# Kernel optimization log

Measured on AMD Instinct MI355X. Metric: run time of the kernel, lower is better.

## Reference

```python
import jax, jax.numpy as jnp
import numpy as np

N, D = 8192, 256
ALPHA, BETA, K = 50.0, 1.0, 2


def setup_inputs() -> dict:
    key = jax.random.key(0)
    k1, k2, k3, k4 = jax.random.split(key, 4)
    Q = jax.random.normal(k1, (N, D), dtype=jnp.float32)
    # 0/1 similarity structure; diagonal forced nonzero so no row is fully masked
    sim = jax.random.randint(k2, (N, N), 0, 2).astype(jnp.float32)
    sim = sim.at[jnp.arange(N), jnp.arange(N)].set(1.0)
    # nn.Linear(in_dim, in_dim) params: y = x @ W.T + b
    bound = 1.0 / np.sqrt(D)
    W = jax.random.uniform(k3, (D, D), jnp.float32, -bound, bound)
    b = jax.random.uniform(k4, (D,), jnp.float32, -bound, bound)
    return {"Q": Q, "sim_mat": sim, "W": W, "b": b}


def reference(Q, sim_mat, W, b):
    mask = sim_mat == 0  # (N, N) bool, constant across iterations
    H = Q
    for _ in range(K):
        H_proj = H @ W.T + b                      # (N, d)
        scores = H_proj @ H_proj.T                # (N, N)
        scores = jnp.where(mask, -jnp.inf, scores)
        lamb = jax.nn.softmax(scores, axis=1)     # (N, N)
        numerator = ALPHA * Q + BETA * (lamb @ H)
        denominator = ALPHA + BETA * jnp.sum(lamb, axis=1, keepdims=True)
        H = numerator / denominator
    return H
```

## Files before the change

kernel.cpp:

```cpp
#include <hip/hip_runtime.h>

#define NN 8192
#define DD 256
#define ALPHA 50.0f
#define BETA 1.0f
#define THR 10.0f
#define KQ 8
#define KEYS (NN / KQ)
#define STEPS (KEYS / 32)
#define QROWS 128

typedef __attribute__((ext_vector_type(8))) short short8;
typedef __attribute__((ext_vector_type(4))) float f32x4;

static __device__ __forceinline__ ushort f2bf(float f) {
    union { float f; unsigned u; } v; v.f = f;
    unsigned u = v.u;
    return (ushort)((u + 0x7fffu + ((u >> 16) & 1u)) >> 16);
}
static __device__ __forceinline__ float bf2f(ushort u) {
    union { unsigned u; float f; } v; v.u = ((unsigned)u) << 16;
    return v.f;
}
static __device__ __forceinline__ void gl_lds16(const ushort* g, ushort* l) {
    __builtin_amdgcn_global_load_lds(
        (const __attribute__((address_space(1))) unsigned int*)g,
        (__attribute__((address_space(3))) unsigned int*)l, 16, 0, 0);
}

__global__ void k_wconv(const float* __restrict__ W, ushort* __restrict__ Wb) {
    int i = blockIdx.x * 256 + threadIdx.x;
    Wb[i] = f2bf(W[i]);
}

__global__ __launch_bounds__(256) void k_pack(const float* __restrict__ sim,
                                              unsigned* __restrict__ bits) {
    __shared__ unsigned char nibs[256];
    int row = blockIdx.x;
    int tid = threadIdx.x;
    for (int p = 0; p < 8; ++p) {
        int col = p * 1024 + tid * 4;
        float4 v = *reinterpret_cast<const float4*>(sim + (size_t)row * NN + col);
        unsigned char nib = (unsigned char)((v.x != 0.f) | ((v.y != 0.f) << 1) |
                                            ((v.z != 0.f) << 2) | ((v.w != 0.f) << 3));
        nibs[tid] = nib;
        __syncthreads();
        if (tid < 32) {
            unsigned word = 0;
#pragma unroll
            for (int i = 0; i < 8; ++i) word |= ((unsigned)nibs[tid * 8 + i]) << (4 * i);
            bits[row * (NN / 32) + p * 32 + tid] = word;
        }
        __syncthreads();
    }
}

__global__ __launch_bounds__(256) void k_convert(const float* __restrict__ H,
                                                 ushort* __restrict__ Hv,
                                                 ushort* __restrict__ Hvt) {
    __shared__ ushort T[64][72];
    int tile = blockIdx.x;
    int r0 = (tile >> 2) * 64;
    int c0 = (tile & 3) * 64;
    int tid = threadIdx.x;
    int tr = tid >> 4;
    int tc = (tid & 15) * 4;
    for (int i = 0; i < 4; ++i) {
        int r = tr + i * 16;
        float4 v = *reinterpret_cast<const float4*>(H + (size_t)(r0 + r) * DD + c0 + tc);
        ushort4 o;
        o.x = f2bf(v.x); o.y = f2bf(v.y); o.z = f2bf(v.z); o.w = f2bf(v.w);
        *reinterpret_cast<ushort4*>(Hv + (size_t)(r0 + r) * DD + c0 + tc) = o;
        T[tc + 0][r] = o.x; T[tc + 1][r] = o.y; T[tc + 2][r] = o.z; T[tc + 3][r] = o.w;
    }
    __syncthreads();
    for (int i = 0; i < 4; ++i) {
        int c = tr + i * 16;
        ushort4 o;
        o.x = T[c][tc + 0]; o.y = T[c][tc + 1]; o.z = T[c][tc + 2]; o.w = T[c][tc + 3];
        *reinterpret_cast<ushort4*>(Hvt + (size_t)(c0 + c) * NN + r0 + tc) = o;
    }
}

__global__ __launch_bounds__(256) void k_proj(const ushort* __restrict__ Hv,
                                              const ushort* __restrict__ Wb,
                                              const float* __restrict__ b,
                                              ushort* __restrict__ Hp) {
    int w = threadIdx.x >> 6;
    int lane = threadIdx.x & 63;
    int row0 = (blockIdx.x >> 1) * 64 + w * 16;
    int ch = blockIdx.x & 1;
    int lr = lane & 15;
    int lk = lane >> 4;
    short8 af[8];
    for (int kk = 0; kk < 8; ++kk)
        af[kk] = *reinterpret_cast<const short8*>(Hv + (size_t)(row0 + lr) * DD + kk * 32 + lk * 8);
    for (int t = 0; t < 8; ++t) {
        f32x4 acc = {0.f, 0.f, 0.f, 0.f};
        int col = (ch * 8 + t) * 16 + lr;
        for (int kk = 0; kk < 8; ++kk) {
            short8 bf = *reinterpret_cast<const short8*>(Wb + (size_t)col * DD + kk * 32 + lk * 8);
            acc = __builtin_amdgcn_mfma_f32_16x16x32_bf16(af[kk], bf, acc, 0, 0, 0);
        }
        float bias = b[col];
        for (int j = 0; j < 4; ++j) {
            int row = row0 + lk * 4 + j;
            Hp[(size_t)row * DD + col] = f2bf(acc[j] + bias);
        }
    }
}

#define PSTR 40
#define SMEM_ATTN (2 * 32 * 256 * 2 + 2 * 256 * 32 * 2 + 8 * 16 * PSTR * 2)
__global__ __launch_bounds__(512) void k_attn(const ushort* __restrict__ Hp,
                                              const ushort* __restrict__ Hvt,
                                              const unsigned* __restrict__ bits,
                                              ushort* __restrict__ Opart,
                                              float* __restrict__ mpart,
                                              float* __restrict__ lpart) {
    extern __shared__ char smem[];
    ushort* KlB = (ushort*)smem;
    ushort* VlB = (ushort*)(smem + 32768);
    ushort* Pl  = (ushort*)(smem + 65536);

    const int tid = threadIdx.x;
    const int w = tid >> 6;
    const int lane = tid & 63;
    const int lr = lane & 15;
    const int lk = lane >> 4;
    const int bid = blockIdx.x;
    const int kq = bid & 7;
    const int qt = bid >> 3;
    const int rw0 = qt * QROWS + w * 16;
    const int kstart = kq * KEYS;

    auto stageK = [&](int buf, int kb) {
        const ushort* Kg = Hp + (size_t)kb * DD;
        ushort* base = KlB + buf * (32 * 256);
#pragma unroll
        for (int i = 0; i < 2; ++i) {
            int S = (w * 2 + i) * 64 + lane;
            int r = S >> 5, cp = S & 31;
            int cc = cp ^ (r & 7);
            gl_lds16(Kg + r * 256 + cc * 8, base + S * 8);
        }
    };
    auto stageV = [&](int buf, int kb) {
        ushort* base = VlB + buf * (256 * 32);
#pragma unroll
        for (int i = 0; i < 2; ++i) {
            int S = (w * 2 + i) * 64 + lane;
            int r = S >> 2, cp = S & 3;
            int cc = cp ^ ((r >> 2) & 3);
            gl_lds16(Hvt + (size_t)r * NN + kb + cc * 8, base + S * 8);
        }
    };

    short8 qf[8];
#pragma unroll
    for (int kk = 0; kk < 8; ++kk)
        qf[kk] = *reinterpret_cast<const short8*>(Hp + (size_t)(rw0 + lr) * DD + kk * 32 + lk * 8);

    f32x4 o[17];
#pragma unroll
    for (int t = 0; t < 17; ++t) o[t] = {0.f, 0.f, 0.f, 0.f};
    float m[4] = {-1e30f, -1e30f, -1e30f, -1e30f};

    short8 ones;
#pragma unroll
    for (int e = 0; e < 8; ++e) ones[e] = (short)0x3f80;

    stageK(0, kstart);
    stageV(0, kstart);
    __syncthreads();

    const int rowbase = (rw0 + lk * 4) * (NN / 32);
    int cur = 0;
    for (int step = 0; step < STEPS; ++step) {
        const int kb = kstart + step * 32;
        if (step + 1 < STEPS) {
            stageK(cur ^ 1, kb + 32);
            stageV(cur ^ 1, kb + 32);
        }
        const int wi = kb >> 5;
        unsigned mwj[4];
#pragma unroll
        for (int j = 0; j < 4; ++j) mwj[j] = bits[rowbase + j * (NN / 32) + wi];

        const char* Kb = (const char*)(KlB + cur * (32 * 256));
        f32x4 s0 = {0.f, 0.f, 0.f, 0.f}, s1 = {0.f, 0.f, 0.f, 0.f};
#pragma unroll
        for (int kk = 0; kk < 8; ++kk) {
            int cp = (kk * 4 + lk) ^ (lr & 7);
            short8 k0 = *reinterpret_cast<const short8*>(Kb + (lr << 9) + (cp << 4));
            short8 k1 = *reinterpret_cast<const short8*>(Kb + ((16 + lr) << 9) + (cp << 4));
            s0 = __builtin_amdgcn_mfma_f32_16x16x32_bf16(qf[kk], k0, s0, 0, 0, 0);
            s1 = __builtin_amdgcn_mfma_f32_16x16x32_bf16(qf[kk], k1, s1, 0, 0, 0);
        }
        float c = -1e30f;
#pragma unroll
        for (int j = 0; j < 4; ++j) {
            float a0 = ((mwj[j] >> lr) & 1u) ? s0[j] : -1e30f;
            float a1 = ((mwj[j] >> (lr + 16)) & 1u) ? s1[j] : -1e30f;
            s0[j] = a0; s1[j] = a1;
            c = fmaxf(c, fmaxf(a0, a1) - m[j]);
        }
        if (__any(c > THR)) {
#pragma unroll
            for (int j = 0; j < 4; ++j) {
                float mx = fmaxf(s0[j], s1[j]);
                mx = fmaxf(mx, __shfl_xor(mx, 1));
                mx = fmaxf(mx, __shfl_xor(mx, 2));
                mx = fmaxf(mx, __shfl_xor(mx, 4));
                mx = fmaxf(mx, __shfl_xor(mx, 8));
                float mn = fmaxf(m[j], mx);
                float scale = __expf(m[j] - mn);
                m[j] = mn;
#pragma unroll
                for (int t = 0; t < 17; ++t) o[t][j] *= scale;
            }
        }
        ushort* Pw = Pl + (size_t)w * 16 * PSTR;
#pragma unroll
        for (int j = 0; j < 4; ++j) {
            Pw[(lk * 4 + j) * PSTR + lr]      = f2bf(__expf(s0[j] - m[j]));
            Pw[(lk * 4 + j) * PSTR + 16 + lr] = f2bf(__expf(s1[j] - m[j]));
        }
        asm volatile("s_waitcnt lgkmcnt(0)" ::: "memory");
        __builtin_amdgcn_sched_barrier(0);
        short8 pa = *reinterpret_cast<const short8*>(Pw + lr * PSTR + lk * 8);
        const char* Vb = (const char*)(VlB + cur * (256 * 32));
        int vcp = lk ^ ((lr >> 2) & 3);
#pragma unroll
        for (int t = 0; t < 16; ++t) {
            short8 vf = *reinterpret_cast<const short8*>(Vb + ((t * 16 + lr) << 6) + (vcp << 4));
            o[t] = __builtin_amdgcn_mfma_f32_16x16x32_bf16(pa, vf, o[t], 0, 0, 0);
        }
        o[16] = __builtin_amdgcn_mfma_f32_16x16x32_bf16(pa, ones, o[16], 0, 0, 0);
        __syncthreads();
        cur ^= 1;
    }

    ushort* op = Opart + ((size_t)kq * NN + rw0) * DD;
#pragma unroll
    for (int t = 0; t < 16; ++t)
#pragma unroll
        for (int j = 0; j < 4; ++j)
            op[(size_t)(lk * 4 + j) * DD + t * 16 + lr] = f2bf(o[t][j]);
    if (lr == 0) {
#pragma unroll
        for (int j = 0; j < 4; ++j) {
            mpart[kq * NN + rw0 + lk * 4 + j] = m[j];
            lpart[kq * NN + rw0 + lk * 4 + j] = o[16][j];
        }
    }
}

__global__ __launch_bounds__(256) void k_merge8(const ushort* __restrict__ Opart,
                                                const float* __restrict__ mpart,
                                                const float* __restrict__ lpart,
                                                const float* __restrict__ Qo,
                                                float* __restrict__ dst) {
    int w = threadIdx.x >> 6;
    int lane = threadIdx.x & 63;
    int r0 = blockIdx.x * 32 + w * 8;
    for (int rr = 0; rr < 8; ++rr) {
        int r = r0 + rr;
        float mv[8], f[8];
        float M = -1e30f;
#pragma unroll
        for (int p = 0; p < 8; ++p) { mv[p] = mpart[p * NN + r]; M = fmaxf(M, mv[p]); }
        float L = 0.f;
#pragma unroll
        for (int p = 0; p < 8; ++p) { f[p] = __expf(mv[p] - M); L += f[p] * lpart[p * NN + r]; }
        float invL = 1.0f / L;
        int c = lane * 4;
        float a0 = 0.f, a1 = 0.f, a2 = 0.f, a3 = 0.f;
#pragma unroll
        for (int p = 0; p < 8; ++p) {
            ushort4 u = *reinterpret_cast<const ushort4*>(Opart + ((size_t)p * NN + r) * DD + c);
            a0 += f[p] * bf2f(u.x); a1 += f[p] * bf2f(u.y);
            a2 += f[p] * bf2f(u.z); a3 += f[p] * bf2f(u.w);
        }
        float4 qv = *reinterpret_cast<const float4*>(Qo + (size_t)r * DD + c);
        float4 ov;
        ov.x = (ALPHA * qv.x + a0 * invL) * (1.0f / (ALPHA + BETA));
        ov.y = (ALPHA * qv.y + a1 * invL) * (1.0f / (ALPHA + BETA));
        ov.z = (ALPHA * qv.z + a2 * invL) * (1.0f / (ALPHA + BETA));
        ov.w = (ALPHA * qv.w + a3 * invL) * (1.0f / (ALPHA + BETA));
        *reinterpret_cast<float4*>(dst + (size_t)r * DD + c) = ov;
    }
}

extern "C" void kernel_launch(void* const* d_in, const int* in_sizes, int n_in,
                              void* d_out, int out_size, void* d_ws, size_t ws_size,
                              hipStream_t stream) {
    const float* Q   = (const float*)d_in[0];
    const float* sim = (const float*)d_in[1];
    const float* W   = (const float*)d_in[2];
    const float* b   = (const float*)d_in[3];
    float* out = (float*)d_out;

    char* ws = (char*)d_ws;
    size_t off = 0;
    ushort* Hv   = (ushort*)(ws + off); off += (size_t)NN * DD * 2;
    ushort* HvtA = (ushort*)(ws + off); off += (size_t)NN * DD * 2;
    ushort* HvtB = (ushort*)(ws + off); off += (size_t)NN * DD * 2;
    ushort* Hp   = (ushort*)(ws + off); off += (size_t)NN * DD * 2;
    ushort* Wb   = (ushort*)(ws + off); off += (size_t)DD * DD * 2;
    unsigned* bits = (unsigned*)(ws + off); off += (size_t)NN * (NN / 32) * 4;
    float*  H1   = (float*)(ws + off);  off += (size_t)NN * DD * 4;
    ushort* Opart = (ushort*)(ws + off); off += (size_t)KQ * NN * DD * 2;
    float*  mpart = (float*)(ws + off);  off += (size_t)KQ * NN * 4;
    float*  lpart = (float*)(ws + off);  off += (size_t)KQ * NN * 4;

    (void)hipFuncSetAttribute((const void*)k_attn,
                              hipFuncAttributeMaxDynamicSharedMemorySize, SMEM_ATTN);

    k_wconv<<<DD * DD / 256, 256, 0, stream>>>(W, Wb);
    k_pack<<<NN, 256, 0, stream>>>(sim, bits);
    k_convert<<<(NN / 64) * (DD / 64), 256, 0, stream>>>(Q, Hv, HvtA);

    k_proj<<<NN / 32, 256, 0, stream>>>(Hv, Wb, b, Hp);
    k_attn<<<(NN / QROWS) * KQ, 512, SMEM_ATTN, stream>>>(Hp, HvtA, bits, Opart, mpart, lpart);
    k_merge8<<<NN / 32, 256, 0, stream>>>(Opart, mpart, lpart, Q, H1);
    k_convert<<<(NN / 64) * (DD / 64), 256, 0, stream>>>(H1, Hv, HvtB);

    k_proj<<<NN / 32, 256, 0, stream>>>(Hv, Wb, b, Hp);
    k_attn<<<(NN / QROWS) * KQ, 512, SMEM_ATTN, stream>>>(Hp, HvtB, bits, Opart, mpart, lpart);
    k_merge8<<<NN / 32, 256, 0, stream>>>(Opart, mpart, lpart, Q, out);
}
```

Before: 359.9 us.

## Process 32 query rows per wave in attention kernel to reuse K/V fragments

Each wave now handles two 16-row query tiles instead of one, so the block shrinks from 512 to 256 threads while still covering 128 query rows. Every K and V fragment read from LDS now feeds two MFMAs, which halves LDS read traffic per MFMA and doubles the per-wave work done between barriers. In exchange, per-thread register use roughly doubles (two O accumulators of 17 vectors each plus two Q fragment sets), which may lower occupancy or cause spills. Fewer waves per block also means less latency hiding.

```diff
diff --git a/kernel.cpp b/kernel.cpp
--- a/kernel.cpp
+++ b/kernel.cpp
@@ -112,7 +112,7 @@
 
 #define PSTR 40
 #define SMEM_ATTN (2 * 32 * 256 * 2 + 2 * 256 * 32 * 2 + 8 * 16 * PSTR * 2)
-__global__ __launch_bounds__(512) void k_attn(const ushort* __restrict__ Hp,
+__global__ __launch_bounds__(256) void k_attn(const ushort* __restrict__ Hp,
                                               const ushort* __restrict__ Hvt,
                                               const unsigned* __restrict__ bits,
                                               ushort* __restrict__ Opart,
@@ -131,15 +131,15 @@
     const int bid = blockIdx.x;
     const int kq = bid & 7;
     const int qt = bid >> 3;
-    const int rw0 = qt * QROWS + w * 16;
+    const int rw0 = qt * QROWS + w * 32;
     const int kstart = kq * KEYS;
 
     auto stageK = [&](int buf, int kb) {
         const ushort* Kg = Hp + (size_t)kb * DD;
         ushort* base = KlB + buf * (32 * 256);
 #pragma unroll
-        for (int i = 0; i < 2; ++i) {
-            int S = (w * 2 + i) * 64 + lane;
+        for (int i = 0; i < 4; ++i) {
+            int S = (w * 4 + i) * 64 + lane;
             int r = S >> 5, cp = S & 31;
             int cc = cp ^ (r & 7);
             gl_lds16(Kg + r * 256 + cc * 8, base + S * 8);
@@ -148,23 +148,26 @@
     auto stageV = [&](int buf, int kb) {
         ushort* base = VlB + buf * (256 * 32);
 #pragma unroll
-        for (int i = 0; i < 2; ++i) {
-            int S = (w * 2 + i) * 64 + lane;
+        for (int i = 0; i < 4; ++i) {
+            int S = (w * 4 + i) * 64 + lane;
             int r = S >> 2, cp = S & 3;
             int cc = cp ^ ((r >> 2) & 3);
             gl_lds16(Hvt + (size_t)r * NN + kb + cc * 8, base + S * 8);
         }
     };
 
-    short8 qf[8];
-#pragma unroll
-    for (int kk = 0; kk < 8; ++kk)
-        qf[kk] = *reinterpret_cast<const short8*>(Hp + (size_t)(rw0 + lr) * DD + kk * 32 + lk * 8);
-
-    f32x4 o[17];
-#pragma unroll
-    for (int t = 0; t < 17; ++t) o[t] = {0.f, 0.f, 0.f, 0.f};
-    float m[4] = {-1e30f, -1e30f, -1e30f, -1e30f};
+    short8 qfA[8], qfB[8];
+#pragma unroll
+    for (int kk = 0; kk < 8; ++kk) {
+        qfA[kk] = *reinterpret_cast<const short8*>(Hp + (size_t)(rw0 + lr) * DD + kk * 32 + lk * 8);
+        qfB[kk] = *reinterpret_cast<const short8*>(Hp + (size_t)(rw0 + 16 + lr) * DD + kk * 32 + lk * 8);
+    }
+
+    f32x4 oA[17], oB[17];
+#pragma unroll
+    for (int t = 0; t < 17; ++t) { oA[t] = {0.f, 0.f, 0.f, 0.f}; oB[t] = {0.f, 0.f, 0.f, 0.f}; }
+    float mA[4] = {-1e30f, -1e30f, -1e30f, -1e30f};
+    float mB[4] = {-1e30f, -1e30f, -1e30f, -1e30f};
 
     short8 ones;
 #pragma unroll
@@ -174,7 +177,10 @@
     stageV(0, kstart);
     __syncthreads();
 
-    const int rowbase = (rw0 + lk * 4) * (NN / 32);
+    const int rbA = (rw0 + lk * 4) * (NN / 32);
+    const int rbB = rbA + 16 * (NN / 32);
+    ushort* PwA = Pl + (size_t)(w * 2) * 16 * PSTR;
+    ushort* PwB = PwA + 16 * PSTR;
     int cur = 0;
     for (int step = 0; step < STEPS; ++step) {
         const int kb = kstart + step * 32;
@@ -183,75 +189,104 @@
             stageV(cur ^ 1, kb + 32);
         }
         const int wi = kb >> 5;
-        unsigned mwj[4];
-#pragma unroll
-        for (int j = 0; j < 4; ++j) mwj[j] = bits[rowbase + j * (NN / 32) + wi];
+        unsigned mwA[4], mwB[4];
+#pragma unroll
+        for (int j = 0; j < 4; ++j) {
+            mwA[j] = bits[rbA + j * (NN / 32) + wi];
+            mwB[j] = bits[rbB + j * (NN / 32) + wi];
+        }
 
         const char* Kb = (const char*)(KlB + cur * (32 * 256));
-        f32x4 s0 = {0.f, 0.f, 0.f, 0.f}, s1 = {0.f, 0.f, 0.f, 0.f};
+        f32x4 s0a = {0.f,0.f,0.f,0.f}, s1a = {0.f,0.f,0.f,0.f};
+        f32x4 s0b = {0.f,0.f,0.f,0.f}, s1b = {0.f,0.f,0.f,0.f};
 #pragma unroll
         for (int kk = 0; kk < 8; ++kk) {
             int cp = (kk * 4 + lk) ^ (lr & 7);
             short8 k0 = *reinterpret_cast<const short8*>(Kb + (lr << 9) + (cp << 4));
             short8 k1 = *reinterpret_cast<const short8*>(Kb + ((16 + lr) << 9) + (cp << 4));
-            s0 = __builtin_amdgcn_mfma_f32_16x16x32_bf16(qf[kk], k0, s0, 0, 0, 0);
-            s1 = __builtin_amdgcn_mfma_f32_16x16x32_bf16(qf[kk], k1, s1, 0, 0, 0);
+            s0a = __builtin_amdgcn_mfma_f32_16x16x32_bf16(qfA[kk], k0, s0a, 0, 0, 0);
+            s0b = __builtin_amdgcn_mfma_f32_16x16x32_bf16(qfB[kk], k0, s0b, 0, 0, 0);
+            s1a = __builtin_amdgcn_mfma_f32_16x16x32_bf16(qfA[kk], k1, s1a, 0, 0, 0);
+            s1b = __builtin_amdgcn_mfma_f32_16x16x32_bf16(qfB[kk], k1, s1b, 0, 0, 0);
         }
         float c = -1e30f;
 #pragma unroll
         for (int j = 0; j < 4; ++j) {
-            float a0 = ((mwj[j] >> lr) & 1u) ? s0[j] : -1e30f;
-            float a1 = ((mwj[j] >> (lr + 16)) & 1u) ? s1[j] : -1e30f;
-            s0[j] = a0; s1[j] = a1;
-            c = fmaxf(c, fmaxf(a0, a1) - m[j]);
+            float a0 = ((mwA[j] >> lr) & 1u) ? s0a[j] : -1e30f;
+            float a1 = ((mwA[j] >> (lr + 16)) & 1u) ? s1a[j] : -1e30f;
+            s0a[j] = a0; s1a[j] = a1;
+            c = fmaxf(c, fmaxf(a0, a1) - mA[j]);
+            float b0 = ((mwB[j] >> lr) & 1u) ? s0b[j] : -1e30f;
+            float b1 = ((mwB[j] >> (lr + 16)) & 1u) ? s1b[j] : -1e30f;
+            s0b[j] = b0; s1b[j] = b1;
+            c = fmaxf(c, fmaxf(b0, b1) - mB[j]);
         }
         if (__any(c > THR)) {
 #pragma unroll
             for (int j = 0; j < 4; ++j) {
-                float mx = fmaxf(s0[j], s1[j]);
+                float mx = fmaxf(s0a[j], s1a[j]);
                 mx = fmaxf(mx, __shfl_xor(mx, 1));
                 mx = fmaxf(mx, __shfl_xor(mx, 2));
                 mx = fmaxf(mx, __shfl_xor(mx, 4));
                 mx = fmaxf(mx, __shfl_xor(mx, 8));
-                float mn = fmaxf(m[j], mx);
-                float scale = __expf(m[j] - mn);
-                m[j] = mn;
-#pragma unroll
-                for (int t = 0; t < 17; ++t) o[t][j] *= scale;
+                float mn = fmaxf(mA[j], mx);
+                float scale = __expf(mA[j] - mn);
+                mA[j] = mn;
+#pragma unroll
+                for (int t = 0; t < 17; ++t) oA[t][j] *= scale;
+                float my = fmaxf(s0b[j], s1b[j]);
+                my = fmaxf(my, __shfl_xor(my, 1));
+                my = fmaxf(my, __shfl_xor(my, 2));
+                my = fmaxf(my, __shfl_xor(my, 4));
+                my = fmaxf(my, __shfl_xor(my, 8));
+                float mn2 = fmaxf(mB[j], my);
+                float scale2 = __expf(mB[j] - mn2);
+                mB[j] = mn2;
+#pragma unroll
+                for (int t = 0; t < 17; ++t) oB[t][j] *= scale2;
             }
         }
-        ushort* Pw = Pl + (size_t)w * 16 * PSTR;
-#pragma unroll
-        for (int j = 0; j < 4; ++j) {
-            Pw[(lk * 4 + j) * PSTR + lr]      = f2bf(__expf(s0[j] - m[j]));
-            Pw[(lk * 4 + j) * PSTR + 16 + lr] = f2bf(__expf(s1[j] - m[j]));
+#pragma unroll
+        for (int j = 0; j < 4; ++j) {
+            PwA[(lk * 4 + j) * PSTR + lr]      = f2bf(__expf(s0a[j] - mA[j]));
+            PwA[(lk * 4 + j) * PSTR + 16 + lr] = f2bf(__expf(s1a[j] - mA[j]));
+            PwB[(lk * 4 + j) * PSTR + lr]      = f2bf(__expf(s0b[j] - mB[j]));
+            PwB[(lk * 4 + j) * PSTR + 16 + lr] = f2bf(__expf(s1b[j] - mB[j]));
         }
         asm volatile("s_waitcnt lgkmcnt(0)" ::: "memory");
         __builtin_amdgcn_sched_barrier(0);
-        short8 pa = *reinterpret_cast<const short8*>(Pw + lr * PSTR + lk * 8);
+        short8 paA = *reinterpret_cast<const short8*>(PwA + lr * PSTR + lk * 8);
+        short8 paB = *reinterpret_cast<const short8*>(PwB + lr * PSTR + lk * 8);
         const char* Vb = (const char*)(VlB + cur * (256 * 32));
         int vcp = lk ^ ((lr >> 2) & 3);
 #pragma unroll
         for (int t = 0; t < 16; ++t) {
             short8 vf = *reinterpret_cast<const short8*>(Vb + ((t * 16 + lr) << 6) + (vcp << 4));
-            o[t] = __builtin_amdgcn_mfma_f32_16x16x32_bf16(pa, vf, o[t], 0, 0, 0);
-        }
-        o[16] = __builtin_amdgcn_mfma_f32_16x16x32_bf16(pa, ones, o[16], 0, 0, 0);
+            oA[t] = __builtin_amdgcn_mfma_f32_16x16x32_bf16(paA, vf, oA[t], 0, 0, 0);
+            oB[t] = __builtin_amdgcn_mfma_f32_16x16x32_bf16(paB, vf, oB[t], 0, 0, 0);
+        }
+        oA[16] = __builtin_amdgcn_mfma_f32_16x16x32_bf16(paA, ones, oA[16], 0, 0, 0);
+        oB[16] = __builtin_amdgcn_mfma_f32_16x16x32_bf16(paB, ones, oB[16], 0, 0, 0);
         __syncthreads();
         cur ^= 1;
     }
 
-    ushort* op = Opart + ((size_t)kq * NN + rw0) * DD;
+    ushort* opA = Opart + ((size_t)kq * NN + rw0) * DD;
+    ushort* opB = opA + (size_t)16 * DD;
 #pragma unroll
     for (int t = 0; t < 16; ++t)
 #pragma unroll
-        for (int j = 0; j < 4; ++j)
-            op[(size_t)(lk * 4 + j) * DD + t * 16 + lr] = f2bf(o[t][j]);
+        for (int j = 0; j < 4; ++j) {
+            opA[(size_t)(lk * 4 + j) * DD + t * 16 + lr] = f2bf(oA[t][j]);
+            opB[(size_t)(lk * 4 + j) * DD + t * 16 + lr] = f2bf(oB[t][j]);
+        }
     if (lr == 0) {
 #pragma unroll
         for (int j = 0; j < 4; ++j) {
-            mpart[kq * NN + rw0 + lk * 4 + j] = m[j];
-            lpart[kq * NN + rw0 + lk * 4 + j] = o[16][j];
+            mpart[kq * NN + rw0 + lk * 4 + j] = mA[j];
+            lpart[kq * NN + rw0 + lk * 4 + j] = oA[16][j];
+            mpart[kq * NN + rw0 + 16 + lk * 4 + j] = mB[j];
+            lpart[kq * NN + rw0 + 16 + lk * 4 + j] = oB[16][j];
         }
     }
 }
@@ -322,11 +357,11 @@
     k_convert<<<(NN / 64) * (DD / 64), 256, 0, stream>>>(Q, Hv, HvtA);
 
     k_proj<<<NN / 32, 256, 0, stream>>>(Hv, Wb, b, Hp);
-    k_attn<<<(NN / QROWS) * KQ, 512, SMEM_ATTN, stream>>>(Hp, HvtA, bits, Opart, mpart, lpart);
+    k_attn<<<(NN / QROWS) * KQ, 256, SMEM_ATTN, stream>>>(Hp, HvtA, bits, Opart, mpart, lpart);
     k_merge8<<<NN / 32, 256, 0, stream>>>(Opart, mpart, lpart, Q, H1);
     k_convert<<<(NN / 64) * (DD / 64), 256, 0, stream>>>(H1, Hv, HvtB);
 
     k_proj<<<NN / 32, 256, 0, stream>>>(Hv, Wb, b, Hp);
-    k_attn<<<(NN / QROWS) * KQ, 512, SMEM_ATTN, stream>>>(Hp, HvtB, bits, Opart, mpart, lpart);
+    k_attn<<<(NN / QROWS) * KQ, 256, SMEM_ATTN, stream>>>(Hp, HvtB, bits, Opart, mpart, lpart);
     k_merge8<<<NN / 32, 256, 0, stream>>>(Opart, mpart, lpart, Q, out);
 }
```

After: 499.3 us. 38.7% more time.
